# Kernel tuning notes

Hardware: AMD Instinct MI355X
Metric: run time of the kernel (lower is better)

Reference implementation:

```python
import jax, jax.numpy as jnp
import numpy as np

N, E, G = 50000, 800000, 200
F_IN, C, HEADS = 16, 64, 4
HID = C * HEADS  # 256


def setup_inputs() -> dict:
    key = jax.random.key(0)
    ks = jax.random.split(key, 30)
    rn = lambda k, s, sc=0.1: jax.random.normal(k, s, jnp.float32) * sc
    inp = {
        'x': jax.random.normal(ks[0], (N, F_IN), jnp.float32),
        'edge_index': jax.random.randint(ks[1], (2, E), 0, N, jnp.int32),
        'batch': jnp.sort(jax.random.randint(ks[2], (N,), 0, G, jnp.int32)),
        'Wl1': rn(ks[3], (F_IN, HID)), 'Wr1': rn(ks[4], (F_IN, HID)),
        'att1': rn(ks[5], (HEADS, C)), 'b1': rn(ks[6], (HID,)),
        'g1': jnp.ones((HID,), jnp.float32), 'be1': jnp.zeros((HID,), jnp.float32),
        'Wl2': rn(ks[7], (HID, HID)), 'Wr2': rn(ks[8], (HID, HID)),
        'att2': rn(ks[9], (HEADS, C)), 'b2': rn(ks[10], (HID,)),
        'g2': jnp.ones((HID,), jnp.float32), 'be2': jnp.zeros((HID,), jnp.float32),
        # GATv2 layer 3: 256 -> 64, 1 head, mean (concat=False)
        'Wl3': rn(ks[11], (HID, C)), 'Wr3': rn(ks[12], (HID, C)),
        'att3': rn(ks[13], (1, C)), 'b3': rn(ks[14], (C,)),
        'g3': jnp.ones((C,), jnp.float32), 'be3': jnp.zeros((C,), jnp.float32),
        # classifier MLP: 128 -> 64 -> 1
        'Wc1': rn(ks[15], (2 * C, C)), 'bc1': rn(ks[16], (C,)),
        'Wc2': rn(ks[17], (C, 1)), 'bc2': rn(ks[18], (1,)),
    }
    return inp


def _gatv2(x, src, dst, Wl, Wr, att, b, heads, c, concat):
    n = x.shape[0]
    xl = (x @ Wl).reshape(n, heads, c)
    xr = (x @ Wr).reshape(n, heads, c)
    s = jax.nn.leaky_relu(xl[src] + xr[dst], 0.2)       # [E', H, C]
    e = jnp.einsum('ehc,hc->eh', s, att)                 # [E', H]
    m = jax.ops.segment_max(e, dst, num_segments=n)
    p = jnp.exp(e - m[dst])
    denom = jax.ops.segment_sum(p, dst, num_segments=n)
    alpha = p / (denom[dst] + 1e-16)
    out = jax.ops.segment_sum(alpha[:, :, None] * xl[src], dst, num_segments=n)
    out = out.reshape(n, heads * c) if concat else out.mean(axis=1)
    return out + b


def _bn(x, g, b):
    mu = x.mean(0)
    v = x.var(0)
    return (x - mu) * jax.lax.rsqrt(v + 1e-5) * g + b


def reference(x, edge_index, batch,
              Wl1, Wr1, att1, b1, g1, be1,
              Wl2, Wr2, att2, b2, g2, be2,
              Wl3, Wr3, att3, b3, g3, be3,
              Wc1, bc1, Wc2, bc2):
    n = x.shape[0]
    loop = jnp.arange(n, dtype=edge_index.dtype)
    src = jnp.concatenate([edge_index[0], loop])  # PyG add_self_loops=True
    dst = jnp.concatenate([edge_index[1], loop])

    h = _gatv2(x, src, dst, Wl1, Wr1, att1, b1, HEADS, C, True)
    h = jax.nn.elu(_bn(h, g1, be1))  # dropout disabled (eval)
    h = _gatv2(h, src, dst, Wl2, Wr2, att2, b2, HEADS, C, True)
    h = jax.nn.elu(_bn(h, g2, be2))
    h = _gatv2(h, src, dst, Wl3, Wr3, att3, b3, 1, C, False)
    h = _bn(h, g3, be3)

    cnt = jax.ops.segment_sum(jnp.ones((n, 1), h.dtype), batch, num_segments=G)
    mean_pool = jax.ops.segment_sum(h, batch, num_segments=G) / jnp.maximum(cnt, 1.0)
    max_pool = jax.ops.segment_max(h, batch, num_segments=G)
    pooled = jnp.concatenate([mean_pool, max_pool], axis=1)  # [G, 128]

    out = jax.nn.relu(pooled @ Wc1 + bc1)
    out = out @ Wc2 + bc2  # [G, 1]
    return out
```

## Files before the change

kernel.cpp:

```cpp
#include <hip/hip_runtime.h>
#include <math.h>

#define N_NODES 50000
#define N_EDGES 800000
#define ET (N_EDGES + N_NODES)
#define N_GRAPHS 200
#define F_INN 16
#define C_DIM 64
#define N_HEADS 4
#define HIDD 256
#define SCAN_BLOCKS ((N_NODES + 255) / 256)

typedef __attribute__((ext_vector_type(8))) short short8;
typedef __attribute__((ext_vector_type(4))) float f32x4;

__device__ __forceinline__ float bf2f(ushort u) {
  return __uint_as_float(((unsigned)u) << 16);
}
__device__ __forceinline__ ushort f2bf(float f) {
  unsigned u = __float_as_uint(f);
  u += 0x7fff + ((u >> 16) & 1);
  return (ushort)(u >> 16);
}

template<int K, int M>
__global__ __launch_bounds__(256) void gemm_dual(
    const float* __restrict__ A, const float* __restrict__ Bl,
    const float* __restrict__ Br, ushort* __restrict__ Clb,
    float* __restrict__ Cr, int nrows)
{
  __shared__ __align__(16) float As[16][64];
  __shared__ __align__(16) float Bls[16][64];
  __shared__ __align__(16) float Brs[16][64];
  int tid = threadIdx.x;
  int row0 = blockIdx.x * 64;
  int col0 = blockIdx.y * 64;
  int tr = (tid >> 4) << 2;
  int tc = (tid & 15) << 2;
  float accL[4][4] = {{0.f}}, accR[4][4] = {{0.f}};
  int arow = tid >> 2, ak = (tid & 3) << 2;
  int brow = tid >> 4, bcol = (tid & 15) << 2;
  for (int k0 = 0; k0 < K; k0 += 16) {
    float4 av = make_float4(0.f, 0.f, 0.f, 0.f);
    int gr = row0 + arow;
    if (gr < nrows) av = *(const float4*)&A[(size_t)gr * K + k0 + ak];
    As[ak + 0][arow] = av.x;
    As[ak + 1][arow] = av.y;
    As[ak + 2][arow] = av.z;
    As[ak + 3][arow] = av.w;
    *(float4*)&Bls[brow][bcol] = *(const float4*)&Bl[(size_t)(k0 + brow) * M + col0 + bcol];
    *(float4*)&Brs[brow][bcol] = *(const float4*)&Br[(size_t)(k0 + brow) * M + col0 + bcol];
    __syncthreads();
    #pragma unroll
    for (int k = 0; k < 16; ++k) {
      float4 a = *(const float4*)&As[k][tr];
      float4 bl = *(const float4*)&Bls[k][tc];
      float4 br = *(const float4*)&Brs[k][tc];
      float aa[4] = {a.x, a.y, a.z, a.w};
      float lb[4] = {bl.x, bl.y, bl.z, bl.w};
      float rb[4] = {br.x, br.y, br.z, br.w};
      #pragma unroll
      for (int ii = 0; ii < 4; ++ii)
        #pragma unroll
        for (int jj = 0; jj < 4; ++jj) {
          accL[ii][jj] = fmaf(aa[ii], lb[jj], accL[ii][jj]);
          accR[ii][jj] = fmaf(aa[ii], rb[jj], accR[ii][jj]);
        }
    }
    __syncthreads();
  }
  #pragma unroll
  for (int ii = 0; ii < 4; ++ii) {
    int gr = row0 + tr + ii;
    if (gr < nrows) {
      *(ushort4*)&Clb[(size_t)gr * M + col0 + tc] =
          make_ushort4(f2bf(accL[ii][0]), f2bf(accL[ii][1]),
                       f2bf(accL[ii][2]), f2bf(accL[ii][3]));
      *(float4*)&Cr[(size_t)gr * M + col0 + tc] =
          make_float4(accR[ii][0], accR[ii][1], accR[ii][2], accR[ii][3]);
    }
  }
}

__device__ __forceinline__ void split_bf16(float a, ushort& hi, ushort& lo) {
  unsigned u = __float_as_uint(a);
  hi = (ushort)(u >> 16);
  float ah = __uint_as_float(u & 0xffff0000u);
  float r = a - ah;
  lo = (ushort)(__float_as_uint(r) >> 16);
}

__global__ __launch_bounds__(256) void convertA(
    const float* __restrict__ H, const float* __restrict__ gsum,
    const float* __restrict__ gsumsq, const float* __restrict__ g,
    const float* __restrict__ be, ushort* __restrict__ Ah,
    ushort* __restrict__ Al, int total4)
{
  int idx = blockIdx.x * blockDim.x + threadIdx.x;
  if (idx >= total4) return;
  int c0 = (idx * 4) & 255;
  float4 v = *(const float4*)&H[(size_t)idx * 4];
  float4 gs4 = *(const float4*)&gsum[c0];
  float4 gq4 = *(const float4*)&gsumsq[c0];
  float4 gg4 = *(const float4*)&g[c0];
  float4 bb4 = *(const float4*)&be[c0];
  const float invn = 1.0f / (float)N_NODES;
  float sc[4], sh[4];
  {
    float gs[4] = {gs4.x, gs4.y, gs4.z, gs4.w};
    float gq[4] = {gq4.x, gq4.y, gq4.z, gq4.w};
    float gg[4] = {gg4.x, gg4.y, gg4.z, gg4.w};
    float bb[4] = {bb4.x, bb4.y, bb4.z, bb4.w};
    #pragma unroll
    for (int j = 0; j < 4; ++j) {
      float mu = gs[j] * invn;
      float var = gq[j] * invn - mu * mu;
      sc[j] = gg[j] * rsqrtf(var + 1e-5f);
      sh[j] = bb[j] - mu * sc[j];
    }
  }
  float t[4] = {fmaf(v.x, sc[0], sh[0]), fmaf(v.y, sc[1], sh[1]),
                fmaf(v.z, sc[2], sh[2]), fmaf(v.w, sc[3], sh[3])};
  ushort hi[4], lo[4];
  #pragma unroll
  for (int j = 0; j < 4; ++j) {
    float e = t[j] > 0.f ? t[j] : __expf(t[j]) - 1.f;
    split_bf16(e, hi[j], lo[j]);
  }
  *(ushort4*)&Ah[(size_t)idx * 4] = make_ushort4(hi[0], hi[1], hi[2], hi[3]);
  *(ushort4*)&Al[(size_t)idx * 4] = make_ushort4(lo[0], lo[1], lo[2], lo[3]);
}

template<int K, int N>
__global__ void convertB(const float* __restrict__ W, ushort* __restrict__ BTmat) {
  int idx = blockIdx.x * blockDim.x + threadIdx.x;
  if (idx >= K * N) return;
  int k = idx / N, n = idx - k * N;
  ushort hi, lo;
  split_bf16(W[idx], hi, lo);
  size_t dst = ((size_t)(k >> 3) * N + n) * 8 + (k & 7);
  BTmat[dst] = hi;
  BTmat[(size_t)(K / 8) * N * 8 + dst] = lo;
}

template<int N>
__global__ __launch_bounds__(256) void gemm_mfma_dual(
    const ushort* __restrict__ Ah, const ushort* __restrict__ Al,
    const ushort* __restrict__ BT, ushort* __restrict__ Clb,
    float* __restrict__ Cr)
{
  constexpr int K = 256;
  constexpr int PLANE = (K / 8) * N * 8;
  const int wave = threadIdx.x >> 6;
  const int lane = threadIdx.x & 63;
  const int r0 = blockIdx.x * 64 + wave * 16;
  const int col0 = blockIdx.y * 64;
  const int kgrp = lane >> 4;
  const int cn = lane & 15;
  const int arow = min(r0 + cn, N_NODES - 1);
  const size_t abase = (size_t)arow * K;
  const ushort* Blh = BT;
  const ushort* Bll = BT + PLANE;
  const ushort* Brh = BT + 2 * PLANE;
  const ushort* Brl = BT + 3 * PLANE;
  f32x4 accL[4], accR[4];
  #pragma unroll
  for (int t = 0; t < 4; ++t) {
    accL[t] = (f32x4)(0.f);
    accR[t] = (f32x4)(0.f);
  }
  #pragma unroll 2
  for (int k0 = 0; k0 < K; k0 += 32) {
    short8 a_h = *(const short8*)&Ah[abase + k0 + kgrp * 8];
    short8 a_l = *(const short8*)&Al[abase + k0 + kgrp * 8];
    const size_t boff = ((size_t)(k0 >> 3) + kgrp) * (N * 8) + (size_t)cn * 8;
    #pragma unroll
    for (int t = 0; t < 4; ++t) {
      const size_t bo = boff + (size_t)(col0 + 16 * t) * 8;
      short8 blh = *(const short8*)&Blh[bo];
      short8 bll = *(const short8*)&Bll[bo];
      short8 brh = *(const short8*)&Brh[bo];
      short8 brl = *(const short8*)&Brl[bo];
      accL[t] = __builtin_amdgcn_mfma_f32_16x16x32_bf16(a_h, blh, accL[t], 0, 0, 0);
      accL[t] = __builtin_amdgcn_mfma_f32_16x16x32_bf16(a_h, bll, accL[t], 0, 0, 0);
      accL[t] = __builtin_amdgcn_mfma_f32_16x16x32_bf16(a_l, blh, accL[t], 0, 0, 0);
      accR[t] = __builtin_amdgcn_mfma_f32_16x16x32_bf16(a_h, brh, accR[t], 0, 0, 0);
      accR[t] = __builtin_amdgcn_mfma_f32_16x16x32_bf16(a_h, brl, accR[t], 0, 0, 0);
      accR[t] = __builtin_amdgcn_mfma_f32_16x16x32_bf16(a_l, brh, accR[t], 0, 0, 0);
    }
  }
  const int crow0 = r0 + kgrp * 4;
  #pragma unroll
  for (int t = 0; t < 4; ++t) {
    int cc = col0 + 16 * t + cn;
    #pragma unroll
    for (int j = 0; j < 4; ++j) {
      int rr = crow0 + j;
      if (rr < N_NODES) {
        Clb[(size_t)rr * N + cc] = f2bf(accL[t][j]);
        Cr[(size_t)rr * N + cc] = accR[t][j];
      }
    }
  }
}

__global__ void hist_kernel(const int* __restrict__ dsts, int* __restrict__ curs) {
  int i = blockIdx.x * blockDim.x + threadIdx.x;
  if (i >= ET) return;
  int d = (i < N_EDGES) ? dsts[i] : i - N_EDGES;
  atomicAdd(&curs[d], 1);
}

__global__ __launch_bounds__(256) void scan_part(
    const int* __restrict__ curs, int* __restrict__ rows, int* __restrict__ bsum)
{
  __shared__ int tmp[256];
  int t = threadIdx.x;
  int i = blockIdx.x * 256 + t;
  int v = (i < N_NODES) ? curs[i] : 0;
  tmp[t] = v;
  __syncthreads();
  #pragma unroll
  for (int off = 1; off < 256; off <<= 1) {
    int u = (t >= off) ? tmp[t - off] : 0;
    __syncthreads();
    tmp[t] += u;
    __syncthreads();
  }
  if (i < N_NODES) rows[i] = tmp[t] - v;
  if (t == 255) bsum[blockIdx.x] = tmp[255];
}

__global__ __launch_bounds__(256) void scan_bsums(
    const int* __restrict__ bsum, int* __restrict__ boff)
{
  __shared__ int tmp[256];
  int t = threadIdx.x;
  int v = (t < SCAN_BLOCKS) ? bsum[t] : 0;
  tmp[t] = v;
  __syncthreads();
  #pragma unroll
  for (int off = 1; off < 256; off <<= 1) {
    int u = (t >= off) ? tmp[t - off] : 0;
    __syncthreads();
    tmp[t] += u;
    __syncthreads();
  }
  if (t < SCAN_BLOCKS) boff[t] = tmp[t] - v;
}

__global__ __launch_bounds__(256) void scan_apply(
    int* __restrict__ rows, const int* __restrict__ boff, int* __restrict__ curs)
{
  int i = blockIdx.x * 256 + threadIdx.x;
  if (i < N_NODES) {
    int r = rows[i] + boff[blockIdx.x];
    rows[i] = r;
    curs[i] = r;
  }
  if (i == 0) rows[N_NODES] = ET;
}

__global__ void scatter_kernel(const int* __restrict__ srcs, const int* __restrict__ dsts,
                               int* __restrict__ curs, int* __restrict__ esrc) {
  int i = blockIdx.x * blockDim.x + threadIdx.x;
  if (i >= ET) return;
  int s, d;
  if (i < N_EDGES) { s = srcs[i]; d = dsts[i]; } else { s = d = i - N_EDGES; }
  int pos = atomicAdd(&curs[d], 1);
  esrc[pos] = s;
}

template<int HEADS_, int D_>
__global__ __launch_bounds__(256) void flash_csr(
    const ushort* __restrict__ xl, const float* __restrict__ xr,
    const float* __restrict__ att, const int* __restrict__ rows,
    const int* __restrict__ esrc, float* __restrict__ out)
{
  int d = blockIdx.x * 4 + (threadIdx.x >> 6);
  if (d >= N_NODES) return;
  int lane = threadIdx.x & 63;
  int beg = rows[d], end = rows[d + 1];
  if constexpr (D_ == 256) {
    float4 xrv = *(const float4*)&xr[(size_t)d * 256 + lane * 4];
    float4 w = *(const float4*)&att[lane * 4];
    auto score = [&](float b0, float b1, float b2, float b3) {
      float v0 = b0 + xrv.x, v1 = b1 + xrv.y, v2 = b2 + xrv.z, v3 = b3 + xrv.w;
      v0 = v0 > 0.f ? v0 : 0.2f * v0;
      v1 = v1 > 0.f ? v1 : 0.2f * v1;
      v2 = v2 > 0.f ? v2 : 0.2f * v2;
      v3 = v3 > 0.f ? v3 : 0.2f * v3;
      return fmaf(v0, w.x, fmaf(v1, w.y, fmaf(v2, w.z, v3 * w.w)));
    };
    float m = -INFINITY, s = 0.f;
    float a0 = 0.f, a1 = 0.f, a2 = 0.f, a3 = 0.f;
    int p = beg;
    for (; p + 4 <= end; p += 4) {
      int s1 = esrc[p], s2 = esrc[p + 1], s3 = esrc[p + 2], s4 = esrc[p + 3];
      ushort4 u1 = *(const ushort4*)&xl[(size_t)s1 * 256 + lane * 4];
      ushort4 u2 = *(const ushort4*)&xl[(size_t)s2 * 256 + lane * 4];
      ushort4 u3 = *(const ushort4*)&xl[(size_t)s3 * 256 + lane * 4];
      ushort4 u4 = *(const ushort4*)&xl[(size_t)s4 * 256 + lane * 4];
      float b10 = bf2f(u1.x), b11 = bf2f(u1.y), b12 = bf2f(u1.z), b13 = bf2f(u1.w);
      float b20 = bf2f(u2.x), b21 = bf2f(u2.y), b22 = bf2f(u2.z), b23 = bf2f(u2.w);
      float b30 = bf2f(u3.x), b31 = bf2f(u3.y), b32 = bf2f(u3.z), b33 = bf2f(u3.w);
      float b40 = bf2f(u4.x), b41 = bf2f(u4.y), b42 = bf2f(u4.z), b43 = bf2f(u4.w);
      float e1 = score(b10, b11, b12, b13);
      float e2 = score(b20, b21, b22, b23);
      float e3 = score(b30, b31, b32, b33);
      float e4 = score(b40, b41, b42, b43);
      e1 += __shfl_xor(e1, 1); e2 += __shfl_xor(e2, 1);
      e3 += __shfl_xor(e3, 1); e4 += __shfl_xor(e4, 1);
      e1 += __shfl_xor(e1, 2); e2 += __shfl_xor(e2, 2);
      e3 += __shfl_xor(e3, 2); e4 += __shfl_xor(e4, 2);
      e1 += __shfl_xor(e1, 4); e2 += __shfl_xor(e2, 4);
      e3 += __shfl_xor(e3, 4); e4 += __shfl_xor(e4, 4);
      e1 += __shfl_xor(e1, 8); e2 += __shfl_xor(e2, 8);
      e3 += __shfl_xor(e3, 8); e4 += __shfl_xor(e4, 8);
      float mn = fmaxf(fmaxf(m, fmaxf(e1, e2)), fmaxf(e3, e4));
      float f = __expf(m - mn);
      float p1 = __expf(e1 - mn);
      float p2 = __expf(e2 - mn);
      float p3 = __expf(e3 - mn);
      float p4 = __expf(e4 - mn);
      s = fmaf(s, f, (p1 + p2) + (p3 + p4));
      a0 = fmaf(a0, f, fmaf(p1, b10, fmaf(p2, b20, fmaf(p3, b30, p4 * b40))));
      a1 = fmaf(a1, f, fmaf(p1, b11, fmaf(p2, b21, fmaf(p3, b31, p4 * b41))));
      a2 = fmaf(a2, f, fmaf(p1, b12, fmaf(p2, b22, fmaf(p3, b32, p4 * b42))));
      a3 = fmaf(a3, f, fmaf(p1, b13, fmaf(p2, b23, fmaf(p3, b33, p4 * b43))));
      m = mn;
    }
    for (; p < end; ++p) {
      int s1 = esrc[p];
      ushort4 u1 = *(const ushort4*)&xl[(size_t)s1 * 256 + lane * 4];
      float b10 = bf2f(u1.x), b11 = bf2f(u1.y), b12 = bf2f(u1.z), b13 = bf2f(u1.w);
      float e1 = score(b10, b11, b12, b13);
      e1 += __shfl_xor(e1, 1);
      e1 += __shfl_xor(e1, 2);
      e1 += __shfl_xor(e1, 4);
      e1 += __shfl_xor(e1, 8);
      float mn = fmaxf(m, e1);
      float f = __expf(m - mn);
      float p1 = __expf(e1 - mn);
      s = fmaf(s, f, p1);
      a0 = fmaf(a0, f, p1 * b10);
      a1 = fmaf(a1, f, p1 * b11);
      a2 = fmaf(a2, f, p1 * b12);
      a3 = fmaf(a3, f, p1 * b13);
      m = mn;
    }
    float inv = 1.f / (s + 1e-16f);
    *(float4*)&out[(size_t)d * 256 + lane * 4] =
        make_float4(a0 * inv, a1 * inv, a2 * inv, a3 * inv);
  } else {
    float xrv = xr[(size_t)d * 64 + lane];
    float w = att[lane];
    float m = -INFINITY, s = 0.f, acc = 0.f;
    int p = beg;
    for (; p + 2 <= end; p += 2) {
      int s1 = esrc[p], s2 = esrc[p + 1];
      float b1 = bf2f(xl[(size_t)s1 * 64 + lane]);
      float b2 = bf2f(xl[(size_t)s2 * 64 + lane]);
      float v1 = b1 + xrv, v2 = b2 + xrv;
      v1 = v1 > 0.f ? v1 : 0.2f * v1;
      v2 = v2 > 0.f ? v2 : 0.2f * v2;
      float e1 = v1 * w, e2 = v2 * w;
      e1 += __shfl_xor(e1, 1);  e2 += __shfl_xor(e2, 1);
      e1 += __shfl_xor(e1, 2);  e2 += __shfl_xor(e2, 2);
      e1 += __shfl_xor(e1, 4);  e2 += __shfl_xor(e2, 4);
      e1 += __shfl_xor(e1, 8);  e2 += __shfl_xor(e2, 8);
      e1 += __shfl_xor(e1, 16); e2 += __shfl_xor(e2, 16);
      e1 += __shfl_xor(e1, 32); e2 += __shfl_xor(e2, 32);
      float mn = fmaxf(m, fmaxf(e1, e2));
      float f = __expf(m - mn);
      float p1 = __expf(e1 - mn);
      float p2 = __expf(e2 - mn);
      s = fmaf(s, f, p1 + p2);
      acc = fmaf(acc, f, fmaf(p1, b1, p2 * b2));
      m = mn;
    }
    if (p < end) {
      int s1 = esrc[p];
      float b1 = bf2f(xl[(size_t)s1 * 64 + lane]);
      float v1 = b1 + xrv;
      v1 = v1 > 0.f ? v1 : 0.2f * v1;
      float e1 = v1 * w;
      e1 += __shfl_xor(e1, 1);
      e1 += __shfl_xor(e1, 2);
      e1 += __shfl_xor(e1, 4);
      e1 += __shfl_xor(e1, 8);
      e1 += __shfl_xor(e1, 16);
      e1 += __shfl_xor(e1, 32);
      float mn = fmaxf(m, e1);
      float f = __expf(m - mn);
      float p1 = __expf(e1 - mn);
      s = fmaf(s, f, p1);
      acc = fmaf(acc, f, p1 * b1);
    }
    out[(size_t)d * 64 + lane] = acc / (s + 1e-16f);
  }
}

template<int D_, int RPB>
__global__ __launch_bounds__(256) void bn_stats(const float* __restrict__ h,
    float* __restrict__ gsum, float* __restrict__ gsumsq, int nrows)
{
  constexpr int RG = 256 / D_;
  int c = threadIdx.x % D_;
  int rg = threadIdx.x / D_;
  int r0 = blockIdx.x * RPB;
  float s = 0.f, sq = 0.f;
  int rend = min(r0 + RPB, nrows);
  for (int r = r0 + rg; r < rend; r += RG) {
    float v = h[(size_t)r * D_ + c];
    s += v;
    sq = fmaf(v, v, sq);
  }
  atomicAdd(&gsum[c], s);
  atomicAdd(&gsumsq[c], sq);
}

__global__ __launch_bounds__(256) void pool_mlp(
    const float* __restrict__ h3, const int* __restrict__ batch,
    const float* __restrict__ gsum, const float* __restrict__ gsumsq,
    const float* __restrict__ g3, const float* __restrict__ be3,
    const float* __restrict__ Wc1, const float* __restrict__ bc1,
    const float* __restrict__ Wc2, const float* __restrict__ bc2,
    float* __restrict__ outp)
{
  int g = blockIdx.x;
  int t = threadIdx.x;
  int lane = t & 63, w = t >> 6;
  int lo, hi;
  {
    int a = 0, b = N_NODES;
    while (a < b) { int mid = (a + b) >> 1; if (batch[mid] < g) a = mid + 1; else b = mid; }
    lo = a;
    b = N_NODES;
    while (a < b) { int mid = (a + b) >> 1; if (batch[mid] < g + 1) a = mid + 1; else b = mid; }
    hi = a;
  }
  const float invn = 1.0f / (float)N_NODES;
  float mu = gsum[lane] * invn;
  float var = gsumsq[lane] * invn - mu * mu;
  float scl = g3[lane] * rsqrtf(var + 1e-5f);
  float shf = be3[lane] - mu * scl;
  float s = 0.f, mx = -INFINITY;
  for (int r = lo + w; r < hi; r += 4) {
    float v = fmaf(h3[(size_t)r * 64 + lane], scl, shf);
    s += v;
    mx = fmaxf(mx, v);
  }
  __shared__ float ssum[4][64];
  __shared__ float smax[4][64];
  __shared__ float pooled[128];
  ssum[w][lane] = s;
  smax[w][lane] = mx;
  __syncthreads();
  if (w == 0) {
    float tot = ssum[0][lane] + ssum[1][lane] + ssum[2][lane] + ssum[3][lane];
    float m4 = fmaxf(fmaxf(smax[0][lane], smax[1][lane]),
                     fmaxf(smax[2][lane], smax[3][lane]));
    float cnt = (float)(hi - lo);
    pooled[lane] = tot / fmaxf(cnt, 1.f);
    pooled[64 + lane] = m4;
  }
  __syncthreads();
  if (w == 0) {
    float a = bc1[lane];
    #pragma unroll 8
    for (int k = 0; k < 128; ++k) a = fmaf(pooled[k], Wc1[k * 64 + lane], a);
    a = fmaxf(a, 0.f);
    float v = a * Wc2[lane];
    v += __shfl_xor(v, 1);
    v += __shfl_xor(v, 2);
    v += __shfl_xor(v, 4);
    v += __shfl_xor(v, 8);
    v += __shfl_xor(v, 16);
    v += __shfl_xor(v, 32);
    if (lane == 0) outp[g] = v + bc2[0];
  }
}

extern "C" void kernel_launch(void* const* d_in, const int* in_sizes, int n_in,
                              void* d_out, int out_size, void* d_ws, size_t ws_size,
                              hipStream_t stream)
{
  const float* x    = (const float*)d_in[0];
  const int*   ei   = (const int*)d_in[1];
  const int*   batch= (const int*)d_in[2];
  const float* Wl1  = (const float*)d_in[3];
  const float* Wr1  = (const float*)d_in[4];
  const float* att1 = (const float*)d_in[5];
  const float* g1   = (const float*)d_in[7];
  const float* be1  = (const float*)d_in[8];
  const float* Wl2  = (const float*)d_in[9];
  const float* Wr2  = (const float*)d_in[10];
  const float* att2 = (const float*)d_in[11];
  const float* g2   = (const float*)d_in[13];
  const float* be2  = (const float*)d_in[14];
  const float* Wl3  = (const float*)d_in[15];
  const float* Wr3  = (const float*)d_in[16];
  const float* att3 = (const float*)d_in[17];
  const float* g3   = (const float*)d_in[19];
  const float* be3  = (const float*)d_in[20];
  const float* Wc1  = (const float*)d_in[21];
  const float* bc1  = (const float*)d_in[22];
  const float* Wc2  = (const float*)d_in[23];
  const float* bc2  = (const float*)d_in[24];

  const int* srcs = ei;
  const int* dsts = ei + N_EDGES;

  float* ws = (float*)d_ws;
  size_t o = 0;
  ushort* XLB = (ushort*)(ws + o); o += (size_t)N_NODES * HIDD / 2;
  float* XR = ws + o;            o += (size_t)N_NODES * HIDD;
  float* Hb = ws + o;            o += (size_t)N_NODES * HIDD;
  ushort* AH = (ushort*)(ws + o); o += (size_t)N_NODES * HIDD / 2;
  ushort* AL = (ushort*)(ws + o); o += (size_t)N_NODES * HIDD / 2;
  ushort* BT2 = (ushort*)(ws + o); o += (size_t)4 * 32 * 256 * 8 / 2;
  ushort* BT3 = (ushort*)(ws + o); o += (size_t)4 * 32 * 64 * 8 / 2;
  int* ESRC = (int*)(ws + o);    o += ET;
  int* ROWS = (int*)(ws + o);    o += N_NODES + 1;
  int* CURS = (int*)(ws + o);    o += N_NODES;
  int* BSUM = (int*)(ws + o);    o += SCAN_BLOCKS;
  int* BOFF = (int*)(ws + o);    o += SCAN_BLOCKS;
  float* GS  = ws + o;           o += 256;
  float* GSQ = ws + o;           o += 256;

  const int ROW_BLOCKS = (N_NODES + 63) / 64;
  const int DST_BLOCKS = (N_NODES + 3) / 4;
  const int A4 = N_NODES * HIDD / 4;
  constexpr int PLANE2 = 32 * 256 * 8;
  constexpr int PLANE3 = 32 * 64 * 8;

  convertB<256, 256><<<(65536 + 255) / 256, 256, 0, stream>>>(Wl2, BT2);
  convertB<256, 256><<<(65536 + 255) / 256, 256, 0, stream>>>(Wr2, BT2 + 2 * PLANE2);
  convertB<256, 64><<<(16384 + 255) / 256, 256, 0, stream>>>(Wl3, BT3);
  convertB<256, 64><<<(16384 + 255) / 256, 256, 0, stream>>>(Wr3, BT3 + 2 * PLANE3);

  hipMemsetAsync(CURS, 0, N_NODES * 4, stream);
  hist_kernel<<<(ET + 255) / 256, 256, 0, stream>>>(dsts, CURS);
  scan_part<<<SCAN_BLOCKS, 256, 0, stream>>>(CURS, ROWS, BSUM);
  scan_bsums<<<1, 256, 0, stream>>>(BSUM, BOFF);
  scan_apply<<<SCAN_BLOCKS, 256, 0, stream>>>(ROWS, BOFF, CURS);
  scatter_kernel<<<(ET + 255) / 256, 256, 0, stream>>>(srcs, dsts, CURS, ESRC);

  gemm_dual<16, 256><<<dim3(ROW_BLOCKS, 4), 256, 0, stream>>>(
      x, Wl1, Wr1, XLB, XR, N_NODES);
  flash_csr<4, 256><<<DST_BLOCKS, 256, 0, stream>>>(XLB, XR, att1, ROWS, ESRC, Hb);
  hipMemsetAsync(GS, 0, 512 * 4, stream);
  bn_stats<256, 64><<<ROW_BLOCKS, 256, 0, stream>>>(Hb, GS, GSQ, N_NODES);

  convertA<<<(A4 + 255) / 256, 256, 0, stream>>>(Hb, GS, GSQ, g1, be1, AH, AL, A4);
  gemm_mfma_dual<256><<<dim3(ROW_BLOCKS, 4), 256, 0, stream>>>(AH, AL, BT2, XLB, XR);
  flash_csr<4, 256><<<DST_BLOCKS, 256, 0, stream>>>(XLB, XR, att2, ROWS, ESRC, Hb);
  hipMemsetAsync(GS, 0, 512 * 4, stream);
  bn_stats<256, 64><<<ROW_BLOCKS, 256, 0, stream>>>(Hb, GS, GSQ, N_NODES);

  convertA<<<(A4 + 255) / 256, 256, 0, stream>>>(Hb, GS, GSQ, g2, be2, AH, AL, A4);
  gemm_mfma_dual<64><<<dim3(ROW_BLOCKS, 1), 256, 0, stream>>>(AH, AL, BT3, XLB, XR);
  flash_csr<1, 64><<<DST_BLOCKS, 256, 0, stream>>>(XLB, XR, att3, ROWS, ESRC, Hb);
  hipMemsetAsync(GS, 0, 512 * 4, stream);
  bn_stats<64, 256><<<(N_NODES + 255) / 256, 256, 0, stream>>>(Hb, GS, GSQ, N_NODES);

  pool_mlp<<<N_GRAPHS, 256, 0, stream>>>(Hb, batch, GS, GSQ, g3, be3,
                                         Wc1, bc1, Wc2, bc2, (float*)d_out);
}
```

Measured before the change: 647.6 us.

## Fuse BN+ELU+bf16 split into MFMA GEMM via swizzled LDS tiles

Removes the separate convertA pass and its global AH/AL buffers. The GEMM block now computes the BN scale and shift, applies ELU and splits values into bf16 hi/lo directly into XOR-swizzled shared memory for a 64-row tile. Each wave computes a 64x64 output tile that reuses the A fragments from LDS across 4 column tiles, and one block covers all columns, so the A tile is built once instead of once per column-block. The cost is 64KB of LDS per block, which limits occupancy, and larger accumulator register pressure.

Measured after the change: 598.6 us. -7.6%, faster.

```diff
diff --git a/kernel.cpp b/kernel.cpp
--- a/kernel.cpp
+++ b/kernel.cpp
@@ -90,47 +90,6 @@
   lo = (ushort)(__float_as_uint(r) >> 16);
 }
 
-__global__ __launch_bounds__(256) void convertA(
-    const float* __restrict__ H, const float* __restrict__ gsum,
-    const float* __restrict__ gsumsq, const float* __restrict__ g,
-    const float* __restrict__ be, ushort* __restrict__ Ah,
-    ushort* __restrict__ Al, int total4)
-{
-  int idx = blockIdx.x * blockDim.x + threadIdx.x;
-  if (idx >= total4) return;
-  int c0 = (idx * 4) & 255;
-  float4 v = *(const float4*)&H[(size_t)idx * 4];
-  float4 gs4 = *(const float4*)&gsum[c0];
-  float4 gq4 = *(const float4*)&gsumsq[c0];
-  float4 gg4 = *(const float4*)&g[c0];
-  float4 bb4 = *(const float4*)&be[c0];
-  const float invn = 1.0f / (float)N_NODES;
-  float sc[4], sh[4];
-  {
-    float gs[4] = {gs4.x, gs4.y, gs4.z, gs4.w};
-    float gq[4] = {gq4.x, gq4.y, gq4.z, gq4.w};
-    float gg[4] = {gg4.x, gg4.y, gg4.z, gg4.w};
-    float bb[4] = {bb4.x, bb4.y, bb4.z, bb4.w};
-    #pragma unroll
-    for (int j = 0; j < 4; ++j) {
-      float mu = gs[j] * invn;
-      float var = gq[j] * invn - mu * mu;
-      sc[j] = gg[j] * rsqrtf(var + 1e-5f);
-      sh[j] = bb[j] - mu * sc[j];
-    }
-  }
-  float t[4] = {fmaf(v.x, sc[0], sh[0]), fmaf(v.y, sc[1], sh[1]),
-                fmaf(v.z, sc[2], sh[2]), fmaf(v.w, sc[3], sh[3])};
-  ushort hi[4], lo[4];
-  #pragma unroll
-  for (int j = 0; j < 4; ++j) {
-    float e = t[j] > 0.f ? t[j] : __expf(t[j]) - 1.f;
-    split_bf16(e, hi[j], lo[j]);
-  }
-  *(ushort4*)&Ah[(size_t)idx * 4] = make_ushort4(hi[0], hi[1], hi[2], hi[3]);
-  *(ushort4*)&Al[(size_t)idx * 4] = make_ushort4(lo[0], lo[1], lo[2], lo[3]);
-}
-
 template<int K, int N>
 __global__ void convertB(const float* __restrict__ W, ushort* __restrict__ BTmat) {
   int idx = blockIdx.x * blockDim.x + threadIdx.x;
@@ -144,61 +103,110 @@
 }
 
 template<int N>
-__global__ __launch_bounds__(256) void gemm_mfma_dual(
-    const ushort* __restrict__ Ah, const ushort* __restrict__ Al,
-    const ushort* __restrict__ BT, ushort* __restrict__ Clb,
-    float* __restrict__ Cr)
-{
-  constexpr int K = 256;
-  constexpr int PLANE = (K / 8) * N * 8;
-  const int wave = threadIdx.x >> 6;
-  const int lane = threadIdx.x & 63;
-  const int r0 = blockIdx.x * 64 + wave * 16;
-  const int col0 = blockIdx.y * 64;
-  const int kgrp = lane >> 4;
-  const int cn = lane & 15;
-  const int arow = min(r0 + cn, N_NODES - 1);
-  const size_t abase = (size_t)arow * K;
-  const ushort* Blh = BT;
-  const ushort* Bll = BT + PLANE;
-  const ushort* Brh = BT + 2 * PLANE;
-  const ushort* Brl = BT + 3 * PLANE;
-  f32x4 accL[4], accR[4];
+__global__ __launch_bounds__(N * 2) void gemm_fused(
+    const float* __restrict__ H, const float* __restrict__ gsum,
+    const float* __restrict__ gsumsq, const float* __restrict__ g,
+    const float* __restrict__ be, const ushort* __restrict__ BT,
+    ushort* __restrict__ Clb, float* __restrict__ Cr)
+{
+  constexpr int THREADS = N * 2;
+  constexpr int PLANE = 32 * N * 8;
+  __shared__ float SCs[256], SHs[256];
+  __shared__ ushort Ah_s[64 * 256];
+  __shared__ ushort Al_s[64 * 256];
+  const int tid = threadIdx.x;
+  const int brow0 = blockIdx.x * 64;
+
+  const float invn = 1.0f / (float)N_NODES;
+  for (int c = tid; c < 256; c += THREADS) {
+    float mu = gsum[c] * invn;
+    float var = gsumsq[c] * invn - mu * mu;
+    float sc = g[c] * rsqrtf(var + 1e-5f);
+    SCs[c] = sc;
+    SHs[c] = be[c] - mu * sc;
+  }
+  __syncthreads();
+
+  for (int gid = tid; gid < 2048; gid += THREADS) {
+    int r = gid >> 5;
+    int ch0 = (gid & 31) * 8;
+    int grow = min(brow0 + r, N_NODES - 1);
+    float4 v0 = *(const float4*)&H[(size_t)grow * 256 + ch0];
+    float4 v1 = *(const float4*)&H[(size_t)grow * 256 + ch0 + 4];
+    float4 sc0 = *(const float4*)&SCs[ch0];
+    float4 sc1 = *(const float4*)&SCs[ch0 + 4];
+    float4 sh0 = *(const float4*)&SHs[ch0];
+    float4 sh1 = *(const float4*)&SHs[ch0 + 4];
+    float vv[8] = {v0.x, v0.y, v0.z, v0.w, v1.x, v1.y, v1.z, v1.w};
+    float scv[8] = {sc0.x, sc0.y, sc0.z, sc0.w, sc1.x, sc1.y, sc1.z, sc1.w};
+    float shv[8] = {sh0.x, sh0.y, sh0.z, sh0.w, sh1.x, sh1.y, sh1.z, sh1.w};
+    short8 hi8, lo8;
+    #pragma unroll
+    for (int j = 0; j < 8; ++j) {
+      float t = fmaf(vv[j], scv[j], shv[j]);
+      float e = t > 0.f ? t : __expf(t) - 1.f;
+      ushort h, l;
+      split_bf16(e, h, l);
+      hi8[j] = (short)h;
+      lo8[j] = (short)l;
+    }
+    int off = r * 512 + ((ch0 * 2) ^ ((r & 7) << 4));
+    *(short8*)((char*)Ah_s + off) = hi8;
+    *(short8*)((char*)Al_s + off) = lo8;
+  }
+  __syncthreads();
+
+  const int wave = tid >> 6, lane = tid & 63;
+  const int cn = lane & 15, kgrp = lane >> 4;
+  const int combc = wave * 64;
+  const bool isR = combc >= N;
+  const ushort* Bh = BT + (isR ? 2 * PLANE : 0);
+  const ushort* Bl_ = Bh + PLANE;
+  const int cb = combc & (N - 1);
+  f32x4 acc[4][4];
   #pragma unroll
-  for (int t = 0; t < 4; ++t) {
-    accL[t] = (f32x4)(0.f);
-    accR[t] = (f32x4)(0.f);
-  }
+  for (int rt = 0; rt < 4; ++rt)
+    #pragma unroll
+    for (int ct = 0; ct < 4; ++ct) acc[rt][ct] = (f32x4)(0.f);
+
   #pragma unroll 2
-  for (int k0 = 0; k0 < K; k0 += 32) {
-    short8 a_h = *(const short8*)&Ah[abase + k0 + kgrp * 8];
-    short8 a_l = *(const short8*)&Al[abase + k0 + kgrp * 8];
-    const size_t boff = ((size_t)(k0 >> 3) + kgrp) * (N * 8) + (size_t)cn * 8;
+  for (int k0 = 0; k0 < 256; k0 += 32) {
+    short8 ah[4], al[4];
     #pragma unroll
-    for (int t = 0; t < 4; ++t) {
-      const size_t bo = boff + (size_t)(col0 + 16 * t) * 8;
-      short8 blh = *(const short8*)&Blh[bo];
-      short8 bll = *(const short8*)&Bll[bo];
-      short8 brh = *(const short8*)&Brh[bo];
-      short8 brl = *(const short8*)&Brl[bo];
-      accL[t] = __builtin_amdgcn_mfma_f32_16x16x32_bf16(a_h, blh, accL[t], 0, 0, 0);
-      accL[t] = __builtin_amdgcn_mfma_f32_16x16x32_bf16(a_h, bll, accL[t], 0, 0, 0);
-      accL[t] = __builtin_amdgcn_mfma_f32_16x16x32_bf16(a_l, blh, accL[t], 0, 0, 0);
-      accR[t] = __builtin_amdgcn_mfma_f32_16x16x32_bf16(a_h, brh, accR[t], 0, 0, 0);
-      accR[t] = __builtin_amdgcn_mfma_f32_16x16x32_bf16(a_h, brl, accR[t], 0, 0, 0);
-      accR[t] = __builtin_amdgcn_mfma_f32_16x16x32_bf16(a_l, brh, accR[t], 0, 0, 0);
-    }
-  }
-  const int crow0 = r0 + kgrp * 4;
+    for (int rt = 0; rt < 4; ++rt) {
+      int row = rt * 16 + cn;
+      int off = row * 512 + (((k0 * 2) + kgrp * 16) ^ ((row & 7) << 4));
+      ah[rt] = *(const short8*)((const char*)Ah_s + off);
+      al[rt] = *(const short8*)((const char*)Al_s + off);
+    }
+    const size_t bbase = (size_t)((k0 >> 3) + kgrp) * (N * 8);
+    #pragma unroll
+    for (int ct = 0; ct < 4; ++ct) {
+      const size_t bo = bbase + (size_t)(cb + ct * 16 + cn) * 8;
+      short8 bh = *(const short8*)&Bh[bo];
+      short8 bl = *(const short8*)&Bl_[bo];
+      #pragma unroll
+      for (int rt = 0; rt < 4; ++rt) {
+        acc[rt][ct] = __builtin_amdgcn_mfma_f32_16x16x32_bf16(ah[rt], bh, acc[rt][ct], 0, 0, 0);
+        acc[rt][ct] = __builtin_amdgcn_mfma_f32_16x16x32_bf16(ah[rt], bl, acc[rt][ct], 0, 0, 0);
+        acc[rt][ct] = __builtin_amdgcn_mfma_f32_16x16x32_bf16(al[rt], bh, acc[rt][ct], 0, 0, 0);
+      }
+    }
+  }
+
   #pragma unroll
-  for (int t = 0; t < 4; ++t) {
-    int cc = col0 + 16 * t + cn;
+  for (int ct = 0; ct < 4; ++ct) {
+    int cc = cb + ct * 16 + cn;
     #pragma unroll
-    for (int j = 0; j < 4; ++j) {
-      int rr = crow0 + j;
-      if (rr < N_NODES) {
-        Clb[(size_t)rr * N + cc] = f2bf(accL[t][j]);
-        Cr[(size_t)rr * N + cc] = accR[t][j];
+    for (int rt = 0; rt < 4; ++rt) {
+      int crow0 = brow0 + rt * 16 + kgrp * 4;
+      #pragma unroll
+      for (int j = 0; j < 4; ++j) {
+        int rr = crow0 + j;
+        if (rr < N_NODES) {
+          if (!isR) Clb[(size_t)rr * N + cc] = f2bf(acc[rt][ct][j]);
+          else      Cr[(size_t)rr * N + cc] = acc[rt][ct][j];
+        }
       }
     }
   }
@@ -517,8 +525,6 @@
   ushort* XLB = (ushort*)(ws + o); o += (size_t)N_NODES * HIDD / 2;
   float* XR = ws + o;            o += (size_t)N_NODES * HIDD;
   float* Hb = ws + o;            o += (size_t)N_NODES * HIDD;
-  ushort* AH = (ushort*)(ws + o); o += (size_t)N_NODES * HIDD / 2;
-  ushort* AL = (ushort*)(ws + o); o += (size_t)N_NODES * HIDD / 2;
   ushort* BT2 = (ushort*)(ws + o); o += (size_t)4 * 32 * 256 * 8 / 2;
   ushort* BT3 = (ushort*)(ws + o); o += (size_t)4 * 32 * 64 * 8 / 2;
   int* ESRC = (int*)(ws + o);    o += ET;
@@ -531,7 +537,6 @@
 
   const int ROW_BLOCKS = (N_NODES + 63) / 64;
   const int DST_BLOCKS = (N_NODES + 3) / 4;
-  const int A4 = N_NODES * HIDD / 4;
   constexpr int PLANE2 = 32 * 256 * 8;
   constexpr int PLANE3 = 32 * 64 * 8;
 
@@ -553,14 +558,14 @@
   hipMemsetAsync(GS, 0, 512 * 4, stream);
   bn_stats<256, 64><<<ROW_BLOCKS, 256, 0, stream>>>(Hb, GS, GSQ, N_NODES);
 
-  convertA<<<(A4 + 255) / 256, 256, 0, stream>>>(Hb, GS, GSQ, g1, be1, AH, AL, A4);
-  gemm_mfma_dual<256><<<dim3(ROW_BLOCKS, 4), 256, 0, stream>>>(AH, AL, BT2, XLB, XR);
+  gemm_fused<256><<<ROW_BLOCKS, 512, 0, stream>>>(
+      Hb, GS, GSQ, g1, be1, BT2, XLB, XR);
   flash_csr<4, 256><<<DST_BLOCKS, 256, 0, stream>>>(XLB, XR, att2, ROWS, ESRC, Hb);
   hipMemsetAsync(GS, 0, 512 * 4, stream);
   bn_stats<256, 64><<<ROW_BLOCKS, 256, 0, stream>>>(Hb, GS, GSQ, N_NODES);
 
-  convertA<<<(A4 + 255) / 256, 256, 0, stream>>>(Hb, GS, GSQ, g2, be2, AH, AL, A4);
-  gemm_mfma_dual<64><<<dim3(ROW_BLOCKS, 1), 256, 0, stream>>>(AH, AL, BT3, XLB, XR);
+  gemm_fused<64><<<ROW_BLOCKS, 128, 0, stream>>>(
+      Hb, GS, GSQ, g2, be2, BT3, XLB, XR);
   flash_csr<1, 64><<<DST_BLOCKS, 256, 0, stream>>>(XLB, XR, att3, ROWS, ESRC, Hb);
   hipMemsetAsync(GS, 0, 512 * 4, stream);
   bn_stats<64, 256><<<(N_NODES + 255) / 256, 256, 0, stream>>>(Hb, GS, GSQ, N_NODES);
```
